# Performance work log

Measured on AMD Instinct MI355X. Metric: run time of the kernel, lower is better.

The kernel has to match this reference:

```python
import jax, jax.numpy as jnp
import numpy as np
import math

B, C, H, W = 16, 512, 32, 32
HEADS = 8
HD = C // HEADS            # 64 head_dim
NFREQ = HD // 4            # 16 (head_dim % 4 == 0)
MAX_FREQ = 128.0
T = H * W                  # 1024 tokens


def _make_so2_mat():
    # make_2dcoord: meshgrid('ij') of arange(H), arange(W) -> [H, W, 2]
    xg, yg = np.meshgrid(np.arange(H, dtype=np.float32), np.arange(W, dtype=np.float32), indexing='ij')
    coord = np.stack([xg, yg], -1)                                   # [H, W, 2]
    freqs = np.exp(np.linspace(0.0, math.log(MAX_FREQ), NFREQ)).astype(np.float32)  # [NFREQ]
    th = coord[..., None, :] * freqs[None, None, :, None]            # [H, W, NFREQ, 2]
    c, s = np.cos(th), np.sin(th)
    # rotation matrices [[c, -s], [s, c]] -> [H, W, NFREQ, 2(dim), 2, 2]
    mat = np.stack([np.stack([c, -s], -1), np.stack([s, c], -1)], -2)
    mat = mat.reshape(H * W, NFREQ * 2, 2, 2)                        # flatten(2,3) then flatten(0,1)
    return jnp.asarray(mat[:, : HD // 2])                            # [T, HD//2, 2, 2]


def setup_inputs() -> dict:
    key = jax.random.key(0)
    ks = jax.random.split(key, 5)
    mat = _make_so2_mat()
    return {
        'x': jax.random.normal(ks[0], (B, C, H, W), dtype=jnp.float32),
        'w_qkv': jax.random.normal(ks[1], (3 * C, C), dtype=jnp.float32) * 0.02,
        'b_qkv': jax.random.normal(ks[2], (3 * C,), dtype=jnp.float32) * 0.02,
        'w_o': jax.random.normal(ks[3], (C, C), dtype=jnp.float32) * 0.02,
        'b_o': jax.random.normal(ks[4], (C,), dtype=jnp.float32) * 0.02,
        'mat_q': mat,
        'mat_k': mat,
        'mat_v': mat,
        'mat_o': jnp.swapaxes(mat, -2, -1),
    }


def _rep_mul(rep, t):
    # rep: [T, HD//2, 2, 2]; t: [B, nh, T, HD] -> per-pair 2x2 rotation
    tb = t.reshape(B, HEADS, T, HD // 2, 2)
    return jnp.einsum('tfij,bntfj->bntfi', rep, tb).reshape(B, HEADS, T, HD)


def _split_heads(t):
    # 'b (c nh) h w -> b nh (h w) c' (c outer, nh inner in channel dim)
    return t.reshape(B, HD, HEADS, T).transpose(0, 2, 3, 1)


def reference(x, w_qkv, b_qkv, w_o, b_o, mat_q, mat_k, mat_v, mat_o):
    # 1x1 conv QKV projection == channel GEMM
    qkv = jnp.einsum('bchw,oc->bohw', x, w_qkv) + b_qkv[None, :, None, None]
    q, k, v = jnp.split(qkv, 3, axis=1)
    q, k, v = map(_split_heads, (q, k, v))                 # [B, nh, T, HD]
    q = _rep_mul(mat_q, q)
    k = _rep_mul(mat_k, k)
    v = _rep_mul(mat_v, v)
    scale = 1.0 / math.sqrt(HD)
    attn = jax.nn.softmax(jnp.einsum('bntd,bnsd->bnts', q, k) * scale, axis=-1)
    o = jnp.einsum('bnts,bnsd->bntd', attn, v)             # [B, nh, T, HD]
    o = _rep_mul(mat_o, o)
    # 'b nh (h w) c -> b (c nh) h w'
    o = o.reshape(B, HEADS, H, W, HD).transpose(0, 4, 1, 2, 3).reshape(B, C, H, W)
    return jnp.einsum('bchw,oc->bohw', o, w_o) + b_o[None, :, None, None]
```

## Files before the change

kernel.cpp:

```cpp
#include <hip/hip_runtime.h>


typedef __bf16 bf16x8 __attribute__((ext_vector_type(8)));
typedef __bf16 bf16x4 __attribute__((ext_vector_type(4)));
typedef float  f32x4  __attribute__((ext_vector_type(4)));

__device__ __forceinline__ f32x4 mfma16(bf16x8 a, bf16x8 b, f32x4 c) {
    return __builtin_amdgcn_mfma_f32_16x16x32_bf16(a, b, c, 0, 0, 0);
}

__device__ __forceinline__ void async16(const void* g, void* l) {
    __builtin_amdgcn_global_load_lds(
        (const __attribute__((address_space(1))) void*)g,
        (__attribute__((address_space(3))) void*)l, 16, 0, 0);
}

__global__ void k_convert_w(const float* __restrict__ wq, const float* __restrict__ wo,
                            __bf16* __restrict__ wqb, __bf16* __restrict__ wob) {
    int i = blockIdx.x * 256 + threadIdx.x;
    if (i < 3 * 512 * 512) wqb[i] = (__bf16)wq[i];
    if (i < 512 * 512) {
        int o = i >> 9, k2 = i & 511;
        int nh = k2 >> 6, hd = k2 & 63;
        wob[i] = (__bf16)wo[o * 512 + hd * 8 + nh];
    }
}

__global__ void k_transpose_x(const float* __restrict__ x, __bf16* __restrict__ xt) {
    __shared__ float tile[32][33];
    const int b  = blockIdx.z;
    const int c0 = blockIdx.y * 32;
    const int t0 = blockIdx.x * 32;
    const int tx = threadIdx.x, ty = threadIdx.y;
    const float* xp = x + ((size_t)b * 512 + c0) * 1024 + t0;
#pragma unroll
    for (int j = 0; j < 4; j++)
        tile[ty + j * 8][tx] = xp[(ty + j * 8) * 1024 + tx];
    __syncthreads();
    __bf16* xo = xt + ((size_t)b * 1024 + t0) * 512 + c0;
#pragma unroll
    for (int j = 0; j < 4; j++)
        xo[(ty + j * 8) * 512 + tx] = (__bf16)tile[tx][ty + j * 8];
}

__global__ __launch_bounds__(256) void k_gemm_qkv(
        const __bf16* __restrict__ A, const __bf16* __restrict__ W,
        const float* __restrict__ bias,
        const float* __restrict__ matq, const float* __restrict__ matk,
        const float* __restrict__ matv,
        __bf16* __restrict__ qd, __bf16* __restrict__ kd, __bf16* __restrict__ vtd)
{
    __shared__ __bf16 As[128][64];
    __shared__ __bf16 Bs[128][64];
    const int tid = threadIdx.x;
    const int m0 = blockIdx.x * 128;
    const int jb = blockIdx.y;
    const int part = jb >> 2;
    const int nh_base = (jb & 3) * 2;
    const int lane = tid & 63, w = tid >> 6;
    const int ln = lane & 15, quad = lane >> 4;
    const int wr = w >> 1, wc = w & 1;

    const int srow = lane >> 3;
    const int scol = (((lane & 7) ^ srow) * 8);

    const __bf16* arow[4];
    const __bf16* brow[4];
#pragma unroll
    for (int jj = 0; jj < 4; jj++) {
        int rr = w * 32 + jj * 8 + srow;
        arow[jj] = &A[(size_t)(m0 + rr) * 512 + scol];
        int o = part * 512 + (rr & 63) * 8 + nh_base + (rr >> 6);
        brow[jj] = &W[(size_t)o * 512 + scol];
    }

    f32x4 acc[4][4] = {};

    for (int k0 = 0; k0 < 512; k0 += 64) {
#pragma unroll
        for (int jj = 0; jj < 4; jj++)
            async16(arow[jj] + k0, &As[w * 32 + jj * 8][0]);
#pragma unroll
        for (int jj = 0; jj < 4; jj++)
            async16(brow[jj] + k0, &Bs[w * 32 + jj * 8][0]);
        __syncthreads();
#pragma unroll
        for (int h = 0; h < 2; h++) {
            bf16x8 af[4], wf[4];
#pragma unroll
            for (int mi = 0; mi < 4; mi++)
                af[mi] = *(const bf16x8*)&As[wr * 64 + mi * 16 + ln][(((h * 4 + quad) ^ (ln & 7)) * 8)];
#pragma unroll
            for (int ni = 0; ni < 4; ni++)
                wf[ni] = *(const bf16x8*)&Bs[wc * 64 + ni * 16 + ln][(((h * 4 + quad) ^ (ln & 7)) * 8)];
#pragma unroll
            for (int mi = 0; mi < 4; mi++)
#pragma unroll
                for (int ni = 0; ni < 4; ni++)
                    acc[mi][ni] = mfma16(af[mi], wf[ni], acc[mi][ni]);
        }
        __syncthreads();
    }

    const int nh = nh_base + wc;
    const int rowbase = m0 + wr * 64;
    const int b  = rowbase >> 10, t0 = rowbase & 1023;
    const int bh = b * 8 + nh;
    const int ip = ln & 1;
    const float2* matp = (const float2*)(part == 0 ? matq : (part == 1 ? matk : matv));
    __bf16* qkdst = (part == 0) ? qd : kd;

#pragma unroll
    for (int ni = 0; ni < 4; ni++) {
        const int hd = ni * 16 + ln;
        const int f  = hd >> 1;
        const float bias_o = bias[part * 512 + hd * 8 + nh];
#pragma unroll
        for (int mi = 0; mi < 4; mi++) {
            const int tq = t0 + mi * 16 + quad * 4;
            if (part < 2) {
#pragma unroll
                for (int r = 0; r < 4; r++) {
                    int t = tq + r;
                    float val = acc[mi][ni][r] + bias_o;
                    float pr  = __shfl_xor(val, 1);
                    float2 mv = matp[((size_t)t * 32 + f) * 2 + ip];
                    float e  = ip ? pr : val;
                    float oo = ip ? val : pr;
                    float rv = mv.x * e + mv.y * oo;
                    qkdst[((size_t)bh * 1024 + t) * 64 + hd] = (__bf16)rv;
                }
            } else {
                __bf16 pack[4];
#pragma unroll
                for (int r = 0; r < 4; r++) {
                    int t = tq + r;
                    float val = acc[mi][ni][r] + bias_o;
                    float pr  = __shfl_xor(val, 1);
                    float2 mv = matp[((size_t)t * 32 + f) * 2 + ip];
                    float e  = ip ? pr : val;
                    float oo = ip ? val : pr;
                    pack[r] = (__bf16)(mv.x * e + mv.y * oo);
                }
                *(uint2*)&vtd[((size_t)bh * 64 + hd) * 1024 + tq] = *(const uint2*)pack;
            }
        }
    }
}

__global__ __launch_bounds__(256) void k_attn(
        const __bf16* __restrict__ q, const __bf16* __restrict__ kk,
        const __bf16* __restrict__ vt, const float* __restrict__ mato,
        __bf16* __restrict__ od)
{
    __shared__ __bf16 Ks[64][64];
    __shared__ __bf16 Vs[64][64];
    __shared__ __bf16 Ps[4][32][64];
    const int bh = blockIdx.x, qt = blockIdx.y;
    const int tid = threadIdx.x, w = tid >> 6, lane = tid & 63;
    const int ln = lane & 15, quad = lane >> 4;
    const int lx = ln & 7;
    const int srow = lane >> 3;
    const int scol = ((lane & 7) ^ srow) * 8;
    const int qr0 = qt * 128 + w * 32;

    bf16x8 qa[2][2];
#pragma unroll
    for (int mi = 0; mi < 2; mi++)
#pragma unroll
        for (int ki = 0; ki < 2; ki++)
            qa[mi][ki] = *(const bf16x8*)&q[((size_t)bh * 1024 + qr0 + mi * 16 + ln) * 64 + ki * 32 + quad * 8];

    const __bf16* kbase = kk + (size_t)bh * 1024 * 64;
    const __bf16* vbase = vt + (size_t)bh * 64 * 1024;

    f32x4 oacc[2][4] = {};
    f32x4 lacc[2] = {};
    const float C_EXP = 0.18033688011112042f;

    bf16x8 ones;
#pragma unroll
    for (int j = 0; j < 8; j++) ones[j] = (__bf16)1.0f;

    for (int st = 0; st < 16; st++) {
#pragma unroll
        for (int i = 0; i < 2; i++) {
            int r0 = w * 16 + i * 8;
            async16(kbase + (size_t)(st * 64 + r0 + srow) * 64 + scol, &Ks[r0][0]);
            async16(vbase + (size_t)(r0 + srow) * 1024 + st * 64 + scol, &Vs[r0][0]);
        }
        __syncthreads();

#pragma unroll
        for (int si = 0; si < 4; si++) {
            bf16x8 kb0 = *(const bf16x8*)&Ks[si * 16 + ln][((quad    ) ^ lx) * 8];
            bf16x8 kb1 = *(const bf16x8*)&Ks[si * 16 + ln][((quad + 4) ^ lx) * 8];
            f32x4 sc[2] = {};
#pragma unroll
            for (int mi = 0; mi < 2; mi++) {
                sc[mi] = mfma16(kb0, qa[mi][0], sc[mi]);
                sc[mi] = mfma16(kb1, qa[mi][1], sc[mi]);
            }
#pragma unroll
            for (int mi = 0; mi < 2; mi++) {
                bf16x4 pk;
#pragma unroll
                for (int r = 0; r < 4; r++)
                    pk[r] = (__bf16)exp2f(sc[mi][r] * C_EXP);
                *(bf16x4*)((char*)&Ps[w][mi * 16 + ln][0]
                           + (((si * 2 + (quad >> 1)) ^ lx) * 16) + (quad & 1) * 8) = pk;
            }
        }

#pragma unroll
        for (int kt = 0; kt < 2; kt++) {
            bf16x8 pa[2];
#pragma unroll
            for (int mi = 0; mi < 2; mi++)
                pa[mi] = *(const bf16x8*)&Ps[w][mi * 16 + ln][((kt * 4 + quad) ^ lx) * 8];
#pragma unroll
            for (int ni = 0; ni < 4; ni++) {
                bf16x8 vb = *(const bf16x8*)&Vs[ni * 16 + ln][((kt * 4 + quad) ^ lx) * 8];
                oacc[0][ni] = mfma16(vb, pa[0], oacc[0][ni]);
                oacc[1][ni] = mfma16(vb, pa[1], oacc[1][ni]);
            }
            lacc[0] = mfma16(ones, pa[0], lacc[0]);
            lacc[1] = mfma16(ones, pa[1], lacc[1]);
        }
        __syncthreads();
    }

    const float4* mo4 = (const float4*)mato;
#pragma unroll
    for (int mi = 0; mi < 2; mi++) {
        const int t = qr0 + mi * 16 + ln;
        const float invl = 1.0f / lacc[mi][0];
#pragma unroll
        for (int ni = 0; ni < 4; ni++) {
            const int hd0 = ni * 16 + quad * 4;
            const int f   = hd0 >> 1;
            float v0 = oacc[mi][ni][0] * invl;
            float v1 = oacc[mi][ni][1] * invl;
            float v2 = oacc[mi][ni][2] * invl;
            float v3 = oacc[mi][ni][3] * invl;
            float4 m1 = mo4[(size_t)t * 32 + f];
            float4 m2 = mo4[(size_t)t * 32 + f + 1];
            __bf16 pk[4];
            pk[0] = (__bf16)(m1.x * v0 + m1.y * v1);
            pk[1] = (__bf16)(m1.z * v0 + m1.w * v1);
            pk[2] = (__bf16)(m2.x * v2 + m2.y * v3);
            pk[3] = (__bf16)(m2.z * v2 + m2.w * v3);
            *(uint2*)&od[((size_t)bh * 1024 + t) * 64 + hd0] = *(const uint2*)pk;
        }
    }
}

__global__ __launch_bounds__(256) void k_gemm_out(
        const __bf16* __restrict__ A, const __bf16* __restrict__ W,
        const float* __restrict__ bias, float* __restrict__ out)
{
    __shared__ __bf16 As[128][64];
    __shared__ __bf16 Bs[128][64];
    const int tid = threadIdx.x;
    const int m0 = blockIdx.x * 128;
    const int n0 = blockIdx.y * 128;
    const int lane = tid & 63, w = tid >> 6;
    const int ln = lane & 15, quad = lane >> 4;
    const int wr = w >> 1, wc = w & 1;

    const int srow = lane >> 3;
    const int scol = (((lane & 7) ^ srow) * 8);

    const int bb = m0 >> 10, t00 = m0 & 1023;

    const __bf16* arow[4];
    const __bf16* brow[4];
#pragma unroll
    for (int jj = 0; jj < 4; jj++) {
        int rr = w * 32 + jj * 8 + srow;
        arow[jj] = &A[((size_t)bb * 8192 + t00 + rr) * 64 + scol];
        brow[jj] = &W[(size_t)(n0 + rr) * 512 + scol];
    }

    f32x4 acc[4][4] = {};

    for (int k0 = 0; k0 < 512; k0 += 64) {
#pragma unroll
        for (int jj = 0; jj < 4; jj++)
            async16(arow[jj] + (size_t)k0 * 1024, &As[w * 32 + jj * 8][0]);
#pragma unroll
        for (int jj = 0; jj < 4; jj++)
            async16(brow[jj] + k0, &Bs[w * 32 + jj * 8][0]);
        __syncthreads();
#pragma unroll
        for (int h = 0; h < 2; h++) {
            bf16x8 af[4], wf[4];
#pragma unroll
            for (int mi = 0; mi < 4; mi++)
                af[mi] = *(const bf16x8*)&As[wr * 64 + mi * 16 + ln][(((h * 4 + quad) ^ (ln & 7)) * 8)];
#pragma unroll
            for (int ni = 0; ni < 4; ni++)
                wf[ni] = *(const bf16x8*)&Bs[wc * 64 + ni * 16 + ln][(((h * 4 + quad) ^ (ln & 7)) * 8)];
#pragma unroll
            for (int mi = 0; mi < 4; mi++)
#pragma unroll
                for (int ni = 0; ni < 4; ni++)
                    acc[mi][ni] = mfma16(af[mi], wf[ni], acc[mi][ni]);
        }
        __syncthreads();
    }

    const int rowbase = m0 + wr * 64;
    const int bb2 = rowbase >> 10, t0 = rowbase & 1023;
#pragma unroll
    for (int ni = 0; ni < 4; ni++) {
        int o = n0 + wc * 64 + ni * 16 + ln;
        float bias_o = bias[o];
#pragma unroll
        for (int mi = 0; mi < 4; mi++) {
            int t = t0 + mi * 16 + quad * 4;
            f32x4 v = acc[mi][ni];
            v[0] += bias_o; v[1] += bias_o; v[2] += bias_o; v[3] += bias_o;
            *(f32x4*)&out[((size_t)bb2 * 512 + o) * 1024 + t] = v;
        }
    }
}

extern "C" void kernel_launch(void* const* d_in, const int* in_sizes, int n_in,
                              void* d_out, int out_size, void* d_ws, size_t ws_size,
                              hipStream_t stream) {
    (void)in_sizes; (void)n_in; (void)out_size; (void)ws_size;
    const float* x     = (const float*)d_in[0];
    const float* w_qkv = (const float*)d_in[1];
    const float* b_qkv = (const float*)d_in[2];
    const float* w_o   = (const float*)d_in[3];
    const float* b_o   = (const float*)d_in[4];
    const float* mat_q = (const float*)d_in[5];
    const float* mat_k = (const float*)d_in[6];
    const float* mat_v = (const float*)d_in[7];
    const float* mat_o = (const float*)d_in[8];
    float* out = (float*)d_out;

    char* p = (char*)d_ws;
    __bf16* wqb = (__bf16*)p;  p += (size_t)3 * 512 * 512 * 2;
    __bf16* wob = (__bf16*)p;  p += (size_t)512 * 512 * 2;
    char* xt_base = p;
    __bf16* xt  = (__bf16*)p;  p += (size_t)16384 * 512 * 2;
    __bf16* qd  = (__bf16*)p;  p += (size_t)128 * 1024 * 64 * 2;
    __bf16* kd  = (__bf16*)p;  p += (size_t)128 * 1024 * 64 * 2;
    __bf16* vtd = (__bf16*)p;  p += (size_t)128 * 64 * 1024 * 2;
    __bf16* od  = (__bf16*)xt_base;

    k_convert_w  <<<dim3(3072),       dim3(256),    0, stream>>>(w_qkv, w_o, wqb, wob);
    k_transpose_x<<<dim3(32, 16, 16), dim3(32, 8),  0, stream>>>(x, xt);
    k_gemm_qkv   <<<dim3(128, 12),    dim3(256),    0, stream>>>(xt, wqb, b_qkv, mat_q, mat_k, mat_v, qd, kd, vtd);
    k_attn       <<<dim3(128, 8),     dim3(256),    0, stream>>>(qd, kd, vtd, mat_o, od);
    k_gemm_out   <<<dim3(128, 4),     dim3(256),    0, stream>>>(od, wob, b_o, out);
}
```

Measured before the change: 240.8 us.

## Double-buffer GEMMs, widen tiles to 512 threads, fold softmax scale into Q

```diff
diff --git a/kernel.cpp b/kernel.cpp
--- a/kernel.cpp
+++ b/kernel.cpp
@@ -27,80 +27,106 @@
 }
 
 __global__ void k_transpose_x(const float* __restrict__ x, __bf16* __restrict__ xt) {
-    __shared__ float tile[32][33];
+    __shared__ float tile[64][65];
     const int b  = blockIdx.z;
-    const int c0 = blockIdx.y * 32;
-    const int t0 = blockIdx.x * 32;
+    const int c0 = blockIdx.y * 64;
+    const int t0 = blockIdx.x * 64;
     const int tx = threadIdx.x, ty = threadIdx.y;
     const float* xp = x + ((size_t)b * 512 + c0) * 1024 + t0;
 #pragma unroll
-    for (int j = 0; j < 4; j++)
-        tile[ty + j * 8][tx] = xp[(ty + j * 8) * 1024 + tx];
+    for (int j = 0; j < 16; j++)
+        tile[ty + j * 4][tx] = xp[(ty + j * 4) * 1024 + tx];
     __syncthreads();
     __bf16* xo = xt + ((size_t)b * 1024 + t0) * 512 + c0;
 #pragma unroll
-    for (int j = 0; j < 4; j++)
-        xo[(ty + j * 8) * 512 + tx] = (__bf16)tile[tx][ty + j * 8];
-}
-
-__global__ __launch_bounds__(256) void k_gemm_qkv(
+    for (int j = 0; j < 16; j++)
+        xo[(ty + j * 4) * 512 + tx] = (__bf16)tile[tx][ty + j * 4];
+}
+
+__global__ __launch_bounds__(512) void k_gemm_qkv(
         const __bf16* __restrict__ A, const __bf16* __restrict__ W,
         const float* __restrict__ bias,
         const float* __restrict__ matq, const float* __restrict__ matk,
         const float* __restrict__ matv,
         __bf16* __restrict__ qd, __bf16* __restrict__ kd, __bf16* __restrict__ vtd)
 {
-    __shared__ __bf16 As[128][64];
-    __shared__ __bf16 Bs[128][64];
+    __shared__ __bf16 As[2][128][64];
+    __shared__ __bf16 Bs[2][256][64];
     const int tid = threadIdx.x;
     const int m0 = blockIdx.x * 128;
     const int jb = blockIdx.y;
-    const int part = jb >> 2;
-    const int nh_base = (jb & 3) * 2;
+    const int part = jb >> 1;
+    const int nh_base = (jb & 1) * 4;
     const int lane = tid & 63, w = tid >> 6;
     const int ln = lane & 15, quad = lane >> 4;
-    const int wr = w >> 1, wc = w & 1;
+    const int wr = w >> 2, wc = w & 3;
 
     const int srow = lane >> 3;
     const int scol = (((lane & 7) ^ srow) * 8);
 
-    const __bf16* arow[4];
+    const __bf16* arow[2];
     const __bf16* brow[4];
+#pragma unroll
+    for (int jj = 0; jj < 2; jj++) {
+        int rr = w * 16 + jj * 8 + srow;
+        arow[jj] = &A[(size_t)(m0 + rr) * 512 + scol];
+    }
 #pragma unroll
     for (int jj = 0; jj < 4; jj++) {
         int rr = w * 32 + jj * 8 + srow;
-        arow[jj] = &A[(size_t)(m0 + rr) * 512 + scol];
         int o = part * 512 + (rr & 63) * 8 + nh_base + (rr >> 6);
         brow[jj] = &W[(size_t)o * 512 + scol];
     }
 
     f32x4 acc[4][4] = {};
 
-    for (int k0 = 0; k0 < 512; k0 += 64) {
-#pragma unroll
-        for (int jj = 0; jj < 4; jj++)
-            async16(arow[jj] + k0, &As[w * 32 + jj * 8][0]);
-#pragma unroll
-        for (int jj = 0; jj < 4; jj++)
-            async16(brow[jj] + k0, &Bs[w * 32 + jj * 8][0]);
-        __syncthreads();
+#define STAGE_QKV(T, BUF)                                                   \
+    do {                                                                    \
+        const int _k0 = (T) * 64;                                           \
+        _Pragma("unroll")                                                   \
+        for (int jj = 0; jj < 2; jj++)                                      \
+            async16(arow[jj] + _k0, &As[BUF][w * 16 + jj * 8][0]);          \
+        _Pragma("unroll")                                                   \
+        for (int jj = 0; jj < 4; jj++)                                      \
+            async16(brow[jj] + _k0, &Bs[BUF][w * 32 + jj * 8][0]);          \
+    } while (0)
+
+    STAGE_QKV(0, 0);
+    STAGE_QKV(1, 1);
+    asm volatile("s_waitcnt vmcnt(6)" ::: "memory");
+    __builtin_amdgcn_s_barrier();
+
+#pragma unroll
+    for (int t = 0; t < 8; ++t) {
+        const int cur = t & 1;
+        bf16x8 af[2][4], wf[2][4];
 #pragma unroll
         for (int h = 0; h < 2; h++) {
-            bf16x8 af[4], wf[4];
 #pragma unroll
             for (int mi = 0; mi < 4; mi++)
-                af[mi] = *(const bf16x8*)&As[wr * 64 + mi * 16 + ln][(((h * 4 + quad) ^ (ln & 7)) * 8)];
+                af[h][mi] = *(const bf16x8*)&As[cur][wr * 64 + mi * 16 + ln][(((h * 4 + quad) ^ (ln & 7)) * 8)];
 #pragma unroll
             for (int ni = 0; ni < 4; ni++)
-                wf[ni] = *(const bf16x8*)&Bs[wc * 64 + ni * 16 + ln][(((h * 4 + quad) ^ (ln & 7)) * 8)];
+                wf[h][ni] = *(const bf16x8*)&Bs[cur][wc * 64 + ni * 16 + ln][(((h * 4 + quad) ^ (ln & 7)) * 8)];
+        }
+        asm volatile("s_waitcnt lgkmcnt(0)" ::: "memory");
+        __builtin_amdgcn_sched_barrier(0);
+        __builtin_amdgcn_s_barrier();
+        if (t < 6) STAGE_QKV(t + 2, cur);
+        __builtin_amdgcn_s_setprio(1);
+#pragma unroll
+        for (int h = 0; h < 2; h++)
 #pragma unroll
             for (int mi = 0; mi < 4; mi++)
 #pragma unroll
                 for (int ni = 0; ni < 4; ni++)
-                    acc[mi][ni] = mfma16(af[mi], wf[ni], acc[mi][ni]);
-        }
-        __syncthreads();
-    }
+                    acc[mi][ni] = mfma16(af[h][mi], wf[h][ni], acc[mi][ni]);
+        __builtin_amdgcn_s_setprio(0);
+        if (t < 6) { asm volatile("s_waitcnt vmcnt(6)" ::: "memory"); }
+        else       { asm volatile("s_waitcnt vmcnt(0)" ::: "memory"); }
+        __builtin_amdgcn_s_barrier();
+    }
+#undef STAGE_QKV
 
     const int nh = nh_base + wc;
     const int rowbase = m0 + wr * 64;
@@ -109,6 +135,7 @@
     const int ip = ln & 1;
     const float2* matp = (const float2*)(part == 0 ? matq : (part == 1 ? matk : matv));
     __bf16* qkdst = (part == 0) ? qd : kd;
+    const float qscale = (part == 0) ? 0.18033688011112042f : 1.0f;
 
 #pragma unroll
     for (int ni = 0; ni < 4; ni++) {
@@ -127,7 +154,7 @@
                     float2 mv = matp[((size_t)t * 32 + f) * 2 + ip];
                     float e  = ip ? pr : val;
                     float oo = ip ? val : pr;
-                    float rv = mv.x * e + mv.y * oo;
+                    float rv = (mv.x * e + mv.y * oo) * qscale;
                     qkdst[((size_t)bh * 1024 + t) * 64 + hd] = (__bf16)rv;
                 }
             } else {
@@ -148,21 +175,21 @@
     }
 }
 
-__global__ __launch_bounds__(256) void k_attn(
+__global__ __launch_bounds__(512) void k_attn(
         const __bf16* __restrict__ q, const __bf16* __restrict__ kk,
         const __bf16* __restrict__ vt, const float* __restrict__ mato,
         __bf16* __restrict__ od)
 {
     __shared__ __bf16 Ks[64][64];
     __shared__ __bf16 Vs[64][64];
-    __shared__ __bf16 Ps[4][32][64];
+    __shared__ __bf16 Ps[8][32][64];
     const int bh = blockIdx.x, qt = blockIdx.y;
     const int tid = threadIdx.x, w = tid >> 6, lane = tid & 63;
     const int ln = lane & 15, quad = lane >> 4;
     const int lx = ln & 7;
     const int srow = lane >> 3;
     const int scol = ((lane & 7) ^ srow) * 8;
-    const int qr0 = qt * 128 + w * 32;
+    const int qr0 = qt * 256 + w * 32;
 
     bf16x8 qa[2][2];
 #pragma unroll
@@ -176,19 +203,14 @@
 
     f32x4 oacc[2][4] = {};
     f32x4 lacc[2] = {};
-    const float C_EXP = 0.18033688011112042f;
 
     bf16x8 ones;
 #pragma unroll
     for (int j = 0; j < 8; j++) ones[j] = (__bf16)1.0f;
 
     for (int st = 0; st < 16; st++) {
-#pragma unroll
-        for (int i = 0; i < 2; i++) {
-            int r0 = w * 16 + i * 8;
-            async16(kbase + (size_t)(st * 64 + r0 + srow) * 64 + scol, &Ks[r0][0]);
-            async16(vbase + (size_t)(r0 + srow) * 1024 + st * 64 + scol, &Vs[r0][0]);
-        }
+        async16(kbase + (size_t)(st * 64 + w * 8 + srow) * 64 + scol, &Ks[w * 8][0]);
+        async16(vbase + (size_t)(w * 8 + srow) * 1024 + st * 64 + scol, &Vs[w * 8][0]);
         __syncthreads();
 
 #pragma unroll
@@ -206,7 +228,7 @@
                 bf16x4 pk;
 #pragma unroll
                 for (int r = 0; r < 4; r++)
-                    pk[r] = (__bf16)exp2f(sc[mi][r] * C_EXP);
+                    pk[r] = (__bf16)exp2f(sc[mi][r]);
                 *(bf16x4*)((char*)&Ps[w][mi * 16 + ln][0]
                            + (((si * 2 + (quad >> 1)) ^ lx) * 16) + (quad & 1) * 8) = pk;
             }
@@ -255,60 +277,86 @@
     }
 }
 
-__global__ __launch_bounds__(256) void k_gemm_out(
+__global__ __launch_bounds__(512) void k_gemm_out(
         const __bf16* __restrict__ A, const __bf16* __restrict__ W,
         const float* __restrict__ bias, float* __restrict__ out)
 {
-    __shared__ __bf16 As[128][64];
-    __shared__ __bf16 Bs[128][64];
+    __shared__ __bf16 As[2][128][64];
+    __shared__ __bf16 Bs[2][256][64];
     const int tid = threadIdx.x;
     const int m0 = blockIdx.x * 128;
-    const int n0 = blockIdx.y * 128;
+    const int n0 = blockIdx.y * 256;
     const int lane = tid & 63, w = tid >> 6;
     const int ln = lane & 15, quad = lane >> 4;
-    const int wr = w >> 1, wc = w & 1;
+    const int wr = w >> 2, wc = w & 3;
 
     const int srow = lane >> 3;
     const int scol = (((lane & 7) ^ srow) * 8);
 
     const int bb = m0 >> 10, t00 = m0 & 1023;
 
-    const __bf16* arow[4];
+    const __bf16* arow[2];
     const __bf16* brow[4];
+#pragma unroll
+    for (int jj = 0; jj < 2; jj++) {
+        int rr = w * 16 + jj * 8 + srow;
+        arow[jj] = &A[((size_t)bb * 8192 + t00 + rr) * 64 + scol];
+    }
 #pragma unroll
     for (int jj = 0; jj < 4; jj++) {
         int rr = w * 32 + jj * 8 + srow;
-        arow[jj] = &A[((size_t)bb * 8192 + t00 + rr) * 64 + scol];
         brow[jj] = &W[(size_t)(n0 + rr) * 512 + scol];
     }
 
     f32x4 acc[4][4] = {};
 
-    for (int k0 = 0; k0 < 512; k0 += 64) {
-#pragma unroll
-        for (int jj = 0; jj < 4; jj++)
-            async16(arow[jj] + (size_t)k0 * 1024, &As[w * 32 + jj * 8][0]);
-#pragma unroll
-        for (int jj = 0; jj < 4; jj++)
-            async16(brow[jj] + k0, &Bs[w * 32 + jj * 8][0]);
-        __syncthreads();
+#define STAGE_OUT(T, BUF)                                                   \
+    do {                                                                    \
+        const int _k0 = (T) * 64;                                           \
+        _Pragma("unroll")                                                   \
+        for (int jj = 0; jj < 2; jj++)                                      \
+            async16(arow[jj] + (size_t)_k0 * 1024, &As[BUF][w * 16 + jj * 8][0]); \
+        _Pragma("unroll")                                                   \
+        for (int jj = 0; jj < 4; jj++)                                      \
+            async16(brow[jj] + _k0, &Bs[BUF][w * 32 + jj * 8][0]);          \
+    } while (0)
+
+    STAGE_OUT(0, 0);
+    STAGE_OUT(1, 1);
+    asm volatile("s_waitcnt vmcnt(6)" ::: "memory");
+    __builtin_amdgcn_s_barrier();
+
+#pragma unroll
+    for (int t = 0; t < 8; ++t) {
+        const int cur = t & 1;
+        bf16x8 af[2][4], wf[2][4];
 #pragma unroll
         for (int h = 0; h < 2; h++) {
-            bf16x8 af[4], wf[4];
 #pragma unroll
             for (int mi = 0; mi < 4; mi++)
-                af[mi] = *(const bf16x8*)&As[wr * 64 + mi * 16 + ln][(((h * 4 + quad) ^ (ln & 7)) * 8)];
+                af[h][mi] = *(const bf16x8*)&As[cur][wr * 64 + mi * 16 + ln][(((h * 4 + quad) ^ (ln & 7)) * 8)];
 #pragma unroll
             for (int ni = 0; ni < 4; ni++)
-                wf[ni] = *(const bf16x8*)&Bs[wc * 64 + ni * 16 + ln][(((h * 4 + quad) ^ (ln & 7)) * 8)];
+                wf[h][ni] = *(const bf16x8*)&Bs[cur][wc * 64 + ni * 16 + ln][(((h * 4 + quad) ^ (ln & 7)) * 8)];
+        }
+        asm volatile("s_waitcnt lgkmcnt(0)" ::: "memory");
+        __builtin_amdgcn_sched_barrier(0);
+        __builtin_amdgcn_s_barrier();
+        if (t < 6) STAGE_OUT(t + 2, cur);
+        __builtin_amdgcn_s_setprio(1);
+#pragma unroll
+        for (int h = 0; h < 2; h++)
 #pragma unroll
             for (int mi = 0; mi < 4; mi++)
 #pragma unroll
                 for (int ni = 0; ni < 4; ni++)
-                    acc[mi][ni] = mfma16(af[mi], wf[ni], acc[mi][ni]);
-        }
-        __syncthreads();
-    }
+                    acc[mi][ni] = mfma16(af[h][mi], wf[h][ni], acc[mi][ni]);
+        __builtin_amdgcn_s_setprio(0);
+        if (t < 6) { asm volatile("s_waitcnt vmcnt(6)" ::: "memory"); }
+        else       { asm volatile("s_waitcnt vmcnt(0)" ::: "memory"); }
+        __builtin_amdgcn_s_barrier();
+    }
+#undef STAGE_OUT
 
     const int rowbase = m0 + wr * 64;
     const int bb2 = rowbase >> 10, t0 = rowbase & 1023;
@@ -352,8 +400,8 @@
     __bf16* od  = (__bf16*)xt_base;
 
     k_convert_w  <<<dim3(3072),       dim3(256),    0, stream>>>(w_qkv, w_o, wqb, wob);
-    k_transpose_x<<<dim3(32, 16, 16), dim3(32, 8),  0, stream>>>(x, xt);
-    k_gemm_qkv   <<<dim3(128, 12),    dim3(256),    0, stream>>>(xt, wqb, b_qkv, mat_q, mat_k, mat_v, qd, kd, vtd);
-    k_attn       <<<dim3(128, 8),     dim3(256),    0, stream>>>(qd, kd, vtd, mat_o, od);
-    k_gemm_out   <<<dim3(128, 4),     dim3(256),    0, stream>>>(od, wob, b_o, out);
-}
+    k_transpose_x<<<dim3(16, 8, 16),  dim3(64, 4),  0, stream>>>(x, xt);
+    k_gemm_qkv   <<<dim3(128, 6),     dim3(512),    0, stream>>>(xt, wqb, b_qkv, mat_q, mat_k, mat_v, qd, kd, vtd);
+    k_attn       <<<dim3(128, 4),     dim3(512),    0, stream>>>(qd, kd, vtd, mat_o, od);
+    k_gemm_out   <<<dim3(128, 2),     dim3(512),    0, stream>>>(od, wob, b_o, out);
+}
```

Result: faster. 223.8 us (-7.1%).
